# Kernel tuning notes

Hardware: AMD Instinct MI355X
Metric: run time of the kernel (lower is better)

## Reference

```python
import jax, jax.numpy as jnp
import numpy as np


def setup_inputs() -> dict:
    key = jax.random.key(0)
    x = jax.random.normal(key, (8, 32, 128, 32, 32), dtype=jnp.float32)
    return {"x": x}


def _gram_schmidt(y):
    # y: [M, C, N, D]; orthogonalize the N vectors (length D) per (M, C)
    n = y.shape[2]
    v0 = y[:, :, 0, :]
    b0 = v0 / jnp.linalg.norm(v0, axis=-1, keepdims=True)
    b0 = jnp.where(jnp.isnan(b0), 0.0, b0)  # torch sets only NaN -> 0
    basis = jnp.zeros_like(y).at[:, :, 0, :].set(b0)

    def step(basis, i):
        v = y[:, :, i, :]                                   # [M, C, D]
        # zero (unfilled) basis rows contribute nothing, so using the full
        # buffer matches the growing-basis math exactly
        coeff = jnp.einsum('mcd,mcnd->mcn', v, basis)       # v . b_j
        proj = jnp.einsum('mcn,mcnd->mcd', coeff, basis)    # sum_j (v.b_j) b_j
        w = v - proj
        wn = w / jnp.linalg.norm(w, axis=-1, keepdims=True)
        wn = jnp.where(jnp.isnan(wn), 0.0, wn)
        return basis.at[:, :, i, :].set(wn), None

    basis, _ = jax.lax.scan(step, basis, jnp.arange(1, n))
    return basis


def reference(x):
    N, M, C, H, W = x.shape
    D = H * W
    y = x.reshape(N, M, C, D).transpose(1, 2, 0, 3)  # [M, C, N, D]
    basis = _gram_schmidt(y)
    # [M, C, N, D] -> [N, M, C, D] -> [N, M, C, H, W]
    return basis.transpose(2, 0, 1, 3).reshape(N, M, C, H, W)
```

## Files before the change

kernel.cpp:

```cpp
#include <hip/hip_runtime.h>


#define MC   4096
#define DIM  1024
#define NV   8
#define TPB  256

__global__ __launch_bounds__(TPB) void gs_kernel(const float* __restrict__ x,
                                                 float* __restrict__ out) {
    const int mc   = blockIdx.x;
    const int t    = threadIdx.x;
    const int lane = t & 63;
    const int wave = t >> 6;

    __shared__ float red[4][NV];

    const size_t strideN = (size_t)MC * DIM;
    const size_t base    = (size_t)mc * DIM + (size_t)t * 4;

    float v[NV][4];
#pragma unroll
    for (int n = 0; n < NV; ++n) {
        const float4 f = *reinterpret_cast<const float4*>(x + n * strideN + base);
        v[n][0] = f.x; v[n][1] = f.y; v[n][2] = f.z; v[n][3] = f.w;
    }

#pragma unroll
    for (int i = 0; i < NV; ++i) {
        if (i > 0) {
            float c[NV];
#pragma unroll
            for (int j = 0; j < NV; ++j) {
                if (j >= i) break;
                float s = v[i][0] * v[j][0] + v[i][1] * v[j][1]
                        + v[i][2] * v[j][2] + v[i][3] * v[j][3];
#pragma unroll
                for (int off = 32; off >= 1; off >>= 1) s += __shfl_xor(s, off, 64);
                if (lane == 0) red[wave][j] = s;
            }
            __syncthreads();
#pragma unroll
            for (int j = 0; j < NV; ++j) {
                if (j >= i) break;
                c[j] = red[0][j] + red[1][j] + red[2][j] + red[3][j];
            }
            __syncthreads();
#pragma unroll
            for (int j = 0; j < NV; ++j) {
                if (j >= i) break;
#pragma unroll
                for (int e = 0; e < 4; ++e) v[i][e] -= c[j] * v[j][e];
            }
        }

        float s = v[i][0] * v[i][0] + v[i][1] * v[i][1]
                + v[i][2] * v[i][2] + v[i][3] * v[i][3];
#pragma unroll
        for (int off = 32; off >= 1; off >>= 1) s += __shfl_xor(s, off, 64);
        if (lane == 0) red[wave][0] = s;
        __syncthreads();
        const float n2 = red[0][0] + red[1][0] + red[2][0] + red[3][0];
        __syncthreads();
        const float rn = (n2 > 0.0f) ? rsqrtf(n2) : 0.0f;
#pragma unroll
        for (int e = 0; e < 4; ++e) v[i][e] *= rn;
    }

#pragma unroll
    for (int n = 0; n < NV; ++n) {
        float4 f;
        f.x = v[n][0]; f.y = v[n][1]; f.z = v[n][2]; f.w = v[n][3];
        *reinterpret_cast<float4*>(out + n * strideN + base) = f;
    }
}

extern "C" void kernel_launch(void* const* d_in, const int* in_sizes, int n_in,
                              void* d_out, int out_size, void* d_ws, size_t ws_size,
                              hipStream_t stream) {
    const float* x = (const float*)d_in[0];
    float* out = (float*)d_out;
    gs_kernel<<<MC, TPB, 0, stream>>>(x, out);
}
```

Before: 249.8 us.

## Replace sequential Gram-Schmidt with Gram matrix plus Cholesky, halve block size

Computes the full 8x8 Gram matrix in a single pass with one batched shuffle reduction and one barrier. A per-thread Cholesky factorisation then yields the projection coefficients and norms, and the vectors are orthonormalised by forward substitution. This removes the many serial reduce-and-sync rounds of classical Gram-Schmidt. Block size drops to 128 threads with 8 elements each, and register use rises. The Cholesky route is numerically less stable for near-dependent vectors, and its handling of degenerate cases differs from the reference's NaN-to-zero behaviour.

```diff
diff --git a/kernel.cpp b/kernel.cpp
--- a/kernel.cpp
+++ b/kernel.cpp
@@ -4,7 +4,9 @@
 #define MC   4096
 #define DIM  1024
 #define NV   8
-#define TPB  256
+#define TPB  128
+#define E    8
+#define IDX(i,j) ((i)*((i)+1)/2+(j))
 
 __global__ __launch_bounds__(TPB) void gs_kernel(const float* __restrict__ x,
                                                  float* __restrict__ out) {
@@ -13,64 +15,99 @@
     const int lane = t & 63;
     const int wave = t >> 6;
 
-    __shared__ float red[4][NV];
+    __shared__ float red[2][36];
 
     const size_t strideN = (size_t)MC * DIM;
-    const size_t base    = (size_t)mc * DIM + (size_t)t * 4;
+    const size_t base    = (size_t)mc * DIM;
 
-    float v[NV][4];
+    float v[NV][E];
 #pragma unroll
     for (int n = 0; n < NV; ++n) {
-        const float4 f = *reinterpret_cast<const float4*>(x + n * strideN + base);
-        v[n][0] = f.x; v[n][1] = f.y; v[n][2] = f.z; v[n][3] = f.w;
+        const float4 a = *reinterpret_cast<const float4*>(x + n * strideN + base + (size_t)t * 4);
+        const float4 b = *reinterpret_cast<const float4*>(x + n * strideN + base + 512 + (size_t)t * 4);
+        v[n][0] = a.x; v[n][1] = a.y; v[n][2] = a.z; v[n][3] = a.w;
+        v[n][4] = b.x; v[n][5] = b.y; v[n][6] = b.z; v[n][7] = b.w;
+    }
+
+    float g[36];
+#pragma unroll
+    for (int i = 0; i < NV; ++i) {
+#pragma unroll
+        for (int j = 0; j <= i; ++j) {
+            float s = 0.0f;
+#pragma unroll
+            for (int e = 0; e < E; ++e) s += v[i][e] * v[j][e];
+            g[IDX(i, j)] = s;
+        }
+    }
+
+#pragma unroll
+    for (int k = 0; k < 36; ++k) {
+        float s = g[k];
+#pragma unroll
+        for (int off = 1; off < 64; off <<= 1) s += __shfl_xor(s, off, 64);
+        g[k] = s;
+    }
+
+    if (lane == 0) {
+#pragma unroll
+        for (int k = 0; k < 36; k += 4) {
+            *reinterpret_cast<float4*>(&red[wave][k]) =
+                make_float4(g[k], g[k + 1], g[k + 2], g[k + 3]);
+        }
+    }
+    __syncthreads();
+#pragma unroll
+    for (int k = 0; k < 36; k += 4) {
+        const float4 a = *reinterpret_cast<const float4*>(&red[0][k]);
+        const float4 b = *reinterpret_cast<const float4*>(&red[1][k]);
+        g[k + 0] = a.x + b.x; g[k + 1] = a.y + b.y;
+        g[k + 2] = a.z + b.z; g[k + 3] = a.w + b.w;
+    }
+
+    float rdiag[NV];
+#pragma unroll
+    for (int i = 0; i < NV; ++i) {
+#pragma unroll
+        for (int j = 0; j < i; ++j) {
+            float s = g[IDX(i, j)];
+#pragma unroll
+            for (int p = 0; p < NV; ++p) {
+                if (p >= j) break;
+                s -= g[IDX(i, p)] * g[IDX(j, p)];
+            }
+            g[IDX(i, j)] = s * rdiag[j];
+        }
+        float d = g[IDX(i, i)];
+#pragma unroll
+        for (int p = 0; p < NV; ++p) {
+            if (p >= i) break;
+            d -= g[IDX(i, p)] * g[IDX(i, p)];
+        }
+        g[IDX(i, i)] = (d > 0.0f) ? sqrtf(d) : 0.0f;
+        rdiag[i]     = (d > 0.0f) ? rsqrtf(d) : 0.0f;
     }
 
 #pragma unroll
     for (int i = 0; i < NV; ++i) {
-        if (i > 0) {
-            float c[NV];
 #pragma unroll
-            for (int j = 0; j < NV; ++j) {
-                if (j >= i) break;
-                float s = v[i][0] * v[j][0] + v[i][1] * v[j][1]
-                        + v[i][2] * v[j][2] + v[i][3] * v[j][3];
+        for (int j = 0; j < NV; ++j) {
+            if (j >= i) break;
+            const float lij = g[IDX(i, j)];
 #pragma unroll
-                for (int off = 32; off >= 1; off >>= 1) s += __shfl_xor(s, off, 64);
-                if (lane == 0) red[wave][j] = s;
-            }
-            __syncthreads();
+            for (int e = 0; e < E; ++e) v[i][e] -= lij * v[j][e];
+        }
+        const float r = rdiag[i];
 #pragma unroll
-            for (int j = 0; j < NV; ++j) {
-                if (j >= i) break;
-                c[j] = red[0][j] + red[1][j] + red[2][j] + red[3][j];
-            }
-            __syncthreads();
-#pragma unroll
-            for (int j = 0; j < NV; ++j) {
-                if (j >= i) break;
-#pragma unroll
-                for (int e = 0; e < 4; ++e) v[i][e] -= c[j] * v[j][e];
-            }
-        }
-
-        float s = v[i][0] * v[i][0] + v[i][1] * v[i][1]
-                + v[i][2] * v[i][2] + v[i][3] * v[i][3];
-#pragma unroll
-        for (int off = 32; off >= 1; off >>= 1) s += __shfl_xor(s, off, 64);
-        if (lane == 0) red[wave][0] = s;
-        __syncthreads();
-        const float n2 = red[0][0] + red[1][0] + red[2][0] + red[3][0];
-        __syncthreads();
-        const float rn = (n2 > 0.0f) ? rsqrtf(n2) : 0.0f;
-#pragma unroll
-        for (int e = 0; e < 4; ++e) v[i][e] *= rn;
+        for (int e = 0; e < E; ++e) v[i][e] *= r;
     }
 
 #pragma unroll
     for (int n = 0; n < NV; ++n) {
-        float4 f;
-        f.x = v[n][0]; f.y = v[n][1]; f.z = v[n][2]; f.w = v[n][3];
-        *reinterpret_cast<float4*>(out + n * strideN + base) = f;
+        *reinterpret_cast<float4*>(out + n * strideN + base + (size_t)t * 4) =
+            make_float4(v[n][0], v[n][1], v[n][2], v[n][3]);
+        *reinterpret_cast<float4*>(out + n * strideN + base + 512 + (size_t)t * 4) =
+            make_float4(v[n][4], v[n][5], v[n][6], v[n][7]);
     }
 }
 
```

New measurement: 244.6 us. 2.1% less time.
